# Kernel optimization log

Measured on AMD Instinct MI355X. Metric: run time of the kernel, lower is better.

Reference implementation:

```python
import jax, jax.numpy as jnp
import numpy as np

B, S, E = 2, 2048, 1024
D_ATTN, H = 1024, 16
HD = D_ATTN // H
SCALE = 1.0 / np.sqrt(D_ATTN)
ROPE_BASE = 10000.0


def setup_inputs() -> dict:
    key = jax.random.key(0)
    ks = jax.random.split(key, 7)
    def w(k, shape, scale):
        return jax.random.normal(k, shape, dtype=jnp.float32) * scale
    return {
        "q": w(ks[0], (B, S, E), 1.0),
        "k": w(ks[1], (B, S, E), 1.0),
        "v": w(ks[2], (B, S, E), 1.0),
        "Wq": w(ks[3], (D_ATTN, E), E ** -0.5),
        "Wk": w(ks[4], (D_ATTN, E), E ** -0.5),
        "Wv": w(ks[5], (D_ATTN, E), E ** -0.5),
        "Wo": w(ks[6], (E, D_ATTN), D_ATTN ** -0.5),
    }


def _rope(x):
    # x: [B, H, S, HD]; interleaved-pair rotary embedding over the seq axis
    s, d = x.shape[2], x.shape[3]
    half = d // 2
    inv_freq = 1.0 / (ROPE_BASE ** (jnp.arange(half, dtype=jnp.float32) * 2.0 / d))
    ang = jnp.arange(s, dtype=jnp.float32)[:, None] * inv_freq[None, :]  # [S, half]
    cos, sin = jnp.cos(ang), jnp.sin(ang)
    xr = x.reshape(x.shape[:-1] + (half, 2))
    x0, x1 = xr[..., 0], xr[..., 1]
    o0 = x0 * cos - x1 * sin
    o1 = x0 * sin + x1 * cos
    return jnp.stack([o0, o1], axis=-1).reshape(x.shape)


def reference(q, k, v, Wq, Wk, Wv, Wo):
    # linear projections (nn.Linear with weight [out, in]): y = x @ W^T
    qh = (q @ Wq.T).reshape(B, S, H, HD).transpose(0, 2, 1, 3)  # [B,H,S,HD]
    kh = (k @ Wk.T).reshape(B, S, H, HD).transpose(0, 2, 1, 3)
    vh = (v @ Wv.T).reshape(B, S, H, HD).transpose(0, 2, 1, 3)
    qh = _rope(qh)
    kh = _rope(kh)
    # shifted-causal mask: disallow j >= i (diagonal masked), except (0,0) allowed
    i = jnp.arange(S)[:, None]
    j = jnp.arange(S)[None, :]
    masked = j >= i                              # triu incl. diagonal
    masked = masked.at[0, 0].set(False)          # keep (0,0) so row 0 isn't all -inf
    scores = jnp.einsum("bhsd,bhtd->bhst", qh, kh) * SCALE
    scores = jnp.where(masked, -jnp.inf, scores)
    probs = jax.nn.softmax(scores, axis=-1)      # dropout omitted (eval mode)
    ctx = jnp.einsum("bhst,bhtd->bhsd", probs, vh)
    ctx = ctx.transpose(0, 2, 1, 3).reshape(B, S, D_ATTN)
    return ctx @ Wo.T
```

## Files before the change

### kernel.cpp

```cpp
#include <hip/hip_runtime.h>
#include <hip/hip_bf16.h>

#define BATCH 2
#define SEQ   2048
#define EMB   1024
#define DATTN 1024
#define NH    16
#define HD    64
#define MM    (BATCH*SEQ)
#define SCALE 0.03125f
#define MINIT -1.0e30f
#define ROPE_COEF 0.41524101186f

using bf16x8 = __attribute__((ext_vector_type(8))) short;
using f32x4  = __attribute__((ext_vector_type(4))) float;

__device__ inline short f2bf(float x) {
    __hip_bfloat16 b = __float2bfloat16(x);
    return *reinterpret_cast<short*>(&b);
}

__device__ inline void gl_lds16(const short* g, short* l) {
    __builtin_amdgcn_global_load_lds(
        (const __attribute__((address_space(1))) unsigned int*)g,
        (__attribute__((address_space(3))) unsigned int*)l, 16, 0, 0);
}

__global__ __launch_bounds__(256)
void cvt_all(const float* __restrict__ q, const float* __restrict__ k,
             const float* __restrict__ v,
             const float* __restrict__ Wq, const float* __restrict__ Wk,
             const float* __restrict__ Wv, const float* __restrict__ Wo,
             short* __restrict__ dst)
{
    const long QKV = (long)MM * EMB;
    const long WSZ = (long)DATTN * EMB;
    const long i = ((long)blockIdx.x * 256 + threadIdx.x) * 4;
    const float* s;
    long off;
    if (i < 3 * QKV) {
        const int seg = (int)(i / QKV);
        off = i - (long)seg * QKV;
        s = (seg == 0) ? q : (seg == 1) ? k : v;
    } else {
        const long j = i - 3 * QKV;
        const int seg = (int)(j / WSZ);
        off = j - (long)seg * WSZ;
        s = (seg == 0) ? Wq : (seg == 1) ? Wk : (seg == 2) ? Wv : Wo;
    }
    float4 x = *(const float4*)(s + off);
    short4 y;
    y.x = f2bf(x.x); y.y = f2bf(x.y); y.z = f2bf(x.z); y.w = f2bf(x.w);
    *(short4*)(dst + i) = y;
}

__device__ inline void stage_tile(const short* g, short* lds, int wave, int lane) {
    #pragma unroll
    for (int qq = 0; qq < 2; ++qq) {
        const int r = wave * 32 + qq * 16 + (lane >> 2);
        gl_lds16(g + (long)r * EMB + (lane & 3) * 8, lds + (wave * 2 + qq) * 512);
    }
}

__device__ inline void stage_tile64(const short* g, short* lds, int tid) {
    #pragma unroll
    for (int c = 0; c < 4; ++c) {
        const int cc   = c * 256 + tid;
        const int row  = cc >> 3;
        const int slot = cc & 7;
        const int ssl  = slot ^ (row & 7);
        gl_lds16(g + (long)row * EMB + ssl * 8, lds + ((cc & ~63) << 3));
    }
}

__global__ __launch_bounds__(256)
void gemm_proj_bf16(const short* __restrict__ qb, const short* __restrict__ kb,
                    const short* __restrict__ vb,
                    const short* __restrict__ wqb, const short* __restrict__ wkb,
                    const short* __restrict__ wvb,
                    short* __restrict__ Qb, short* __restrict__ Kb,
                    short* __restrict__ Vtb)
{
    const short* A; const short* B;
    if (blockIdx.z == 0)      { A = qb; B = wqb; }
    else if (blockIdx.z == 1) { A = kb; B = wkb; }
    else                      { A = vb; B = wvb; }
    const bool isv = (blockIdx.z == 2);

    __shared__ short sA[128 * 64];
    __shared__ short sB[128 * 64];

    const int tid  = threadIdx.x;
    const int wave = tid >> 6, lane = tid & 63;
    const int quad = lane >> 4, l16 = lane & 15;
    const int wm = (wave >> 1) * 64, wn = (wave & 1) * 64;
    const long m0 = (long)blockIdx.x * 128, n0 = (long)blockIdx.y * 128;
    const int rsw = l16 & 7;

    f32x4 acc[4][4];
    #pragma unroll
    for (int i = 0; i < 4; ++i)
        #pragma unroll
        for (int j = 0; j < 4; ++j) acc[i][j] = (f32x4){0.f, 0.f, 0.f, 0.f};

    for (int kt = 0; kt < EMB; kt += 64) {
        __syncthreads();
        stage_tile64(A + m0 * EMB + kt, sA, tid);
        stage_tile64(B + n0 * EMB + kt, sB, tid);
        __syncthreads();

        #pragma unroll
        for (int kk = 0; kk < 2; ++kk) {
            bf16x8 af[4], bfr[4];
            #pragma unroll
            for (int rt = 0; rt < 4; ++rt)
                af[rt] = *(const bf16x8*)&sA[(wm + rt * 16 + l16) * 64
                         + (((kk << 2) | quad) ^ rsw) * 8];
            #pragma unroll
            for (int ct = 0; ct < 4; ++ct)
                bfr[ct] = *(const bf16x8*)&sB[(wn + ct * 16 + l16) * 64
                          + (((kk << 2) | quad) ^ rsw) * 8];
            if (isv) {
                #pragma unroll
                for (int i = 0; i < 4; ++i)
                    #pragma unroll
                    for (int j = 0; j < 4; ++j)
                        acc[i][j] = __builtin_amdgcn_mfma_f32_16x16x32_bf16(
                            af[i], bfr[j], acc[i][j], 0, 0, 0);
            } else {
                #pragma unroll
                for (int i = 0; i < 4; ++i)
                    #pragma unroll
                    for (int j = 0; j < 4; ++j)
                        acc[i][j] = __builtin_amdgcn_mfma_f32_16x16x32_bf16(
                            bfr[i], af[j], acc[i][j], 0, 0, 0);
            }
        }
    }

    if (!isv) {
        short* C = (blockIdx.z == 0) ? Qb : Kb;
        const float scl = (blockIdx.z == 0) ? SCALE : 1.0f;
        #pragma unroll
        for (int i = 0; i < 4; ++i) {
            const int d0  = (int)(n0) + wn + i * 16 + quad * 4;
            const int hh  = d0 >> 6, dd0 = d0 & (HD - 1);
            const float invf0 = exp2f(-ROPE_COEF * (float)(dd0 >> 1));
            const float invf1 = exp2f(-ROPE_COEF * (float)((dd0 >> 1) + 1));
            #pragma unroll
            for (int j = 0; j < 4; ++j) {
                const int tok = (int)(m0) + wm + j * 16 + l16;
                const int bb = tok >> 11, ss = tok & (SEQ - 1);
                float s0, c0, s1, c1;
                __sincosf((float)ss * invf0, &s0, &c0);
                __sincosf((float)ss * invf1, &s1, &c1);
                const f32x4 x = acc[i][j];
                short4 o4;
                o4.x = f2bf((x[0] * c0 - x[1] * s0) * scl);
                o4.y = f2bf((x[0] * s0 + x[1] * c0) * scl);
                o4.z = f2bf((x[2] * c1 - x[3] * s1) * scl);
                o4.w = f2bf((x[2] * s1 + x[3] * c1) * scl);
                *(short4*)&C[(((long)(bb * NH + hh)) << 17)
                             + ((long)ss << 6) + dd0] = o4;
            }
        }
    } else {
        #pragma unroll
        for (int rt = 0; rt < 4; ++rt) {
            #pragma unroll
            for (int ct = 0; ct < 4; ++ct) {
                const long row0 = m0 + wm + rt * 16 + quad * 4;
                const long col  = n0 + wn + ct * 16 + l16;
                const int bb = (int)(row0 >> 11), ss = (int)(row0 & (SEQ - 1));
                const int hh = (int)(col >> 6),   dd = (int)(col & (HD - 1));
                short4 s4;
                s4.x = f2bf(acc[rt][ct][0]); s4.y = f2bf(acc[rt][ct][1]);
                s4.z = f2bf(acc[rt][ct][2]); s4.w = f2bf(acc[rt][ct][3]);
                *(short4*)&Vtb[(((long)(bb * NH + hh)) << 17) + ((long)dd << 11) + ss] = s4;
            }
        }
    }
}

__global__ __launch_bounds__(256)
void gemm_out_bf16(const short* __restrict__ Ab, const short* __restrict__ Bb,
                   float* __restrict__ C)
{
    __shared__ short sA[128 * 32];
    __shared__ short sB[64 * 32];

    const int tid  = threadIdx.x;
    const int wave = tid >> 6, lane = tid & 63;
    const int quad = lane >> 4, l16 = lane & 15;
    const int wm = (wave >> 1) * 64, wn = (wave & 1) * 32;
    const long m0 = (long)blockIdx.x * 128, n0 = (long)blockIdx.y * 64;

    f32x4 acc[4][2];
    #pragma unroll
    for (int i = 0; i < 4; ++i)
        #pragma unroll
        for (int j = 0; j < 2; ++j) acc[i][j] = (f32x4){0.f, 0.f, 0.f, 0.f};

    for (int kt = 0; kt < DATTN; kt += 32) {
        __syncthreads();
        stage_tile(Ab + m0 * DATTN + kt, sA, wave, lane);
        gl_lds16(Bb + n0 * DATTN + kt
                     + (long)(wave * 16 + (lane >> 2)) * DATTN + (lane & 3) * 8,
                 sB + wave * 512);
        __syncthreads();

        bf16x8 af[4], bfr[2];
        #pragma unroll
        for (int rt = 0; rt < 4; ++rt)
            af[rt] = *(const bf16x8*)&sA[(wm + rt * 16 + l16) * 32 + quad * 8];
        #pragma unroll
        for (int ct = 0; ct < 2; ++ct)
            bfr[ct] = *(const bf16x8*)&sB[(wn + ct * 16 + l16) * 32 + quad * 8];
        #pragma unroll
        for (int rt = 0; rt < 4; ++rt)
            #pragma unroll
            for (int ct = 0; ct < 2; ++ct)
                acc[rt][ct] = __builtin_amdgcn_mfma_f32_16x16x32_bf16(
                    af[rt], bfr[ct], acc[rt][ct], 0, 0, 0);
    }

    #pragma unroll
    for (int rt = 0; rt < 4; ++rt) {
        #pragma unroll
        for (int ct = 0; ct < 2; ++ct) {
            #pragma unroll
            for (int reg = 0; reg < 4; ++reg) {
                const long row = m0 + wm + rt * 16 + quad * 4 + reg;
                const long col = n0 + wn + ct * 16 + l16;
                C[row * EMB + col] = acc[rt][ct][reg];
            }
        }
    }
}

#define KLD 64
#define PLD 72

__global__ __launch_bounds__(256, 2)
void flash_attn_mfma(const short* __restrict__ Qb,
                     const short* __restrict__ Kb,
                     const short* __restrict__ Vtb,
                     short* __restrict__ ctx)
{
    const int id  = blockIdx.x;
    const int hi  = id >> 8;
    const int idx = id & 255;
    const int r   = idx & 7;
    const int s5  = idx >> 3;
    const int pi  = s5 & 3;
    const int ts8 = s5 >> 2;
    const int p   = r + 8 * pi;
    const int b   = p >> 4, h = p & 15;
    const int t   = hi ? ts8 : (15 - ts8);

    const int tid = threadIdx.x;
    const int wave = tid >> 6, lane = tid & 63;
    const int quad = lane >> 4, l16 = lane & 15;
    const int r0 = t * 128;

    __shared__ short sk[2 * 64 * KLD];
    __shared__ short sv[2 * 64 * KLD];
    __shared__ short sp[4][32 * PLD];

    const long base = ((long)(b * NH + h)) << 17;

    const int iq0 = r0 + wave * 32 + l16;
    const int iq1 = iq0 + 16;
    const int dtile = 2 * t + (wave >> 1);
    const int rsw = l16 & 7;

    bf16x8 qf0[2], qf1[2];
    #pragma unroll
    for (int tt = 0; tt < 2; ++tt) {
        qf0[tt] = *(const bf16x8*)(Qb + base + (long)iq0 * HD + tt * 32 + quad * 8);
        qf1[tt] = *(const bf16x8*)(Qb + base + (long)iq1 * HD + tt * 32 + quad * 8);
    }

    f32x4 acc0[4], acc1[4];
    #pragma unroll
    for (int ct = 0; ct < 4; ++ct) {
        acc0[ct] = (f32x4){0.f, 0.f, 0.f, 0.f};
        acc1[ct] = (f32x4){0.f, 0.f, 0.f, 0.f};
    }
    float m0 = MINIT, l0 = 0.f;
    float m1 = MINIT, l1 = 0.f;

    const int njt = t + 1;

    #pragma unroll 1
    for (int jt = 0; jt < njt; ++jt) {
        const int jbase = jt * 128;

        __syncthreads();
        #pragma unroll
        for (int c = 0; c < 4; ++c) {
            const int cc   = c * 256 + tid;
            const int half = cc >> 9;
            const int row  = (cc >> 3) & 63;
            const int sch  = (cc & 7) ^ (row & 7);
            gl_lds16(Kb + base + (long)(jbase + half * 64 + row) * HD + sch * 8,
                     sk + ((c * 256 + wave * 64) << 3));
            gl_lds16(Vtb + base + ((long)row << 11) + jbase + half * 64 + sch * 8,
                     sv + ((c * 256 + wave * 64) << 3));
        }
        __syncthreads();

        #pragma unroll
        for (int half = 0; half < 2; ++half) {
            const int jt2 = 2 * jt + half;
            if (jt2 > dtile) continue;
            const int jb2 = jbase + half * 64;
            const short* skh = sk + half * 64 * KLD;
            const short* svh = sv + half * 64 * KLD;

            f32x4 s0[4], s1[4];
            __builtin_amdgcn_s_setprio(1);
            #pragma unroll
            for (int ct = 0; ct < 4; ++ct) {
                const int rr16 = (ct * 16 + l16) * KLD;
                bf16x8 k0 = *(const bf16x8*)&skh[rr16 + ((quad ^ rsw) << 3)];
                bf16x8 k1 = *(const bf16x8*)&skh[rr16 + (((4 + quad) ^ rsw) << 3)];
                f32x4 z0 = (f32x4){0.f, 0.f, 0.f, 0.f};
                z0 = __builtin_amdgcn_mfma_f32_16x16x32_bf16(k0, qf0[0], z0, 0, 0, 0);
                z0 = __builtin_amdgcn_mfma_f32_16x16x32_bf16(k1, qf0[1], z0, 0, 0, 0);
                s0[ct] = z0;
                f32x4 z1 = (f32x4){0.f, 0.f, 0.f, 0.f};
                z1 = __builtin_amdgcn_mfma_f32_16x16x32_bf16(k0, qf1[0], z1, 0, 0, 0);
                z1 = __builtin_amdgcn_mfma_f32_16x16x32_bf16(k1, qf1[1], z1, 0, 0, 0);
                s1[ct] = z1;
            }
            __builtin_amdgcn_s_setprio(0);

            if (jt2 == dtile) {
                #pragma unroll
                for (int ct = 0; ct < 4; ++ct)
                    #pragma unroll
                    for (int rr = 0; rr < 4; ++rr) {
                        const int j = jb2 + ct * 16 + quad * 4 + rr;
                        if (!((j < iq0) || (iq0 == 0 && j == 0)))
                            s0[ct][rr] = -INFINITY;
                        if (!(j < iq1))
                            s1[ct][rr] = -INFINITY;
                    }
            }

            float mx0 = MINIT;
            #pragma unroll
            for (int ct = 0; ct < 4; ++ct)
                #pragma unroll
                for (int rr = 0; rr < 4; ++rr) mx0 = fmaxf(mx0, s0[ct][rr]);
            mx0 = fmaxf(mx0, __shfl_xor(mx0, 16, 64));
            mx0 = fmaxf(mx0, __shfl_xor(mx0, 32, 64));
            const float mn0 = fmaxf(m0, mx0);
            const float a0 = __expf(m0 - mn0);
            m0 = mn0;
            float ss0 = 0.f;
            #pragma unroll
            for (int ct = 0; ct < 4; ++ct)
                #pragma unroll
                for (int rr = 0; rr < 4; ++rr) {
                    const float e = __expf(s0[ct][rr] - mn0);
                    s0[ct][rr] = e;
                    ss0 += e;
                }
            ss0 += __shfl_xor(ss0, 16, 64);
            ss0 += __shfl_xor(ss0, 32, 64);
            l0 = l0 * a0 + ss0;

            float mx1 = MINIT;
            #pragma unroll
            for (int ct = 0; ct < 4; ++ct)
                #pragma unroll
                for (int rr = 0; rr < 4; ++rr) mx1 = fmaxf(mx1, s1[ct][rr]);
            mx1 = fmaxf(mx1, __shfl_xor(mx1, 16, 64));
            mx1 = fmaxf(mx1, __shfl_xor(mx1, 32, 64));
            const float mn1 = fmaxf(m1, mx1);
            const float a1 = __expf(m1 - mn1);
            m1 = mn1;
            float ss1 = 0.f;
            #pragma unroll
            for (int ct = 0; ct < 4; ++ct)
                #pragma unroll
                for (int rr = 0; rr < 4; ++rr) {
                    const float e = __expf(s1[ct][rr] - mn1);
                    s1[ct][rr] = e;
                    ss1 += e;
                }
            ss1 += __shfl_xor(ss1, 16, 64);
            ss1 += __shfl_xor(ss1, 32, 64);
            l1 = l1 * a1 + ss1;

            short* pw0 = sp[wave];
            short* pw1 = sp[wave] + 16 * PLD;
            #pragma unroll
            for (int ct = 0; ct < 4; ++ct) {
                short4 p4;
                p4.x = f2bf(s0[ct][0]); p4.y = f2bf(s0[ct][1]);
                p4.z = f2bf(s0[ct][2]); p4.w = f2bf(s0[ct][3]);
                *(short4*)&pw0[l16 * PLD + ct * 16 + quad * 4] = p4;
                short4 q4;
                q4.x = f2bf(s1[ct][0]); q4.y = f2bf(s1[ct][1]);
                q4.z = f2bf(s1[ct][2]); q4.w = f2bf(s1[ct][3]);
                *(short4*)&pw1[l16 * PLD + ct * 16 + quad * 4] = q4;
            }

            #pragma unroll
            for (int ct = 0; ct < 4; ++ct)
                #pragma unroll
                for (int rr = 0; rr < 4; ++rr) {
                    acc0[ct][rr] *= a0;
                    acc1[ct][rr] *= a1;
                }

            bf16x8 pf00 = *(const bf16x8*)&pw0[l16 * PLD + quad * 8];
            bf16x8 pf01 = *(const bf16x8*)&pw0[l16 * PLD + 32 + quad * 8];
            bf16x8 pf10 = *(const bf16x8*)&pw1[l16 * PLD + quad * 8];
            bf16x8 pf11 = *(const bf16x8*)&pw1[l16 * PLD + 32 + quad * 8];

            __builtin_amdgcn_s_setprio(1);
            #pragma unroll
            for (int ct = 0; ct < 4; ++ct) {
                const int rr16 = (ct * 16 + l16) * KLD;
                bf16x8 v0 = *(const bf16x8*)&svh[rr16 + ((quad ^ rsw) << 3)];
                bf16x8 v1 = *(const bf16x8*)&svh[rr16 + (((4 + quad) ^ rsw) << 3)];
                acc0[ct] = __builtin_amdgcn_mfma_f32_16x16x32_bf16(
                    v0, pf00, acc0[ct], 0, 0, 0);
                acc0[ct] = __builtin_amdgcn_mfma_f32_16x16x32_bf16(
                    v1, pf01, acc0[ct], 0, 0, 0);
                acc1[ct] = __builtin_amdgcn_mfma_f32_16x16x32_bf16(
                    v0, pf10, acc1[ct], 0, 0, 0);
                acc1[ct] = __builtin_amdgcn_mfma_f32_16x16x32_bf16(
                    v1, pf11, acc1[ct], 0, 0, 0);
            }
            __builtin_amdgcn_s_setprio(0);
        }
    }

    {
        const float inv0 = 1.f / l0;
        short* orow = ctx + (long)(b * SEQ + iq0) * DATTN + h * HD;
        #pragma unroll
        for (int ct = 0; ct < 4; ++ct) {
            short4 o4;
            o4.x = f2bf(acc0[ct][0] * inv0);
            o4.y = f2bf(acc0[ct][1] * inv0);
            o4.z = f2bf(acc0[ct][2] * inv0);
            o4.w = f2bf(acc0[ct][3] * inv0);
            *(short4*)&orow[ct * 16 + quad * 4] = o4;
        }
    }
    {
        const float inv1 = 1.f / l1;
        short* orow = ctx + (long)(b * SEQ + iq1) * DATTN + h * HD;
        #pragma unroll
        for (int ct = 0; ct < 4; ++ct) {
            short4 o4;
            o4.x = f2bf(acc1[ct][0] * inv1);
            o4.y = f2bf(acc1[ct][1] * inv1);
            o4.z = f2bf(acc1[ct][2] * inv1);
            o4.w = f2bf(acc1[ct][3] * inv1);
            *(short4*)&orow[ct * 16 + quad * 4] = o4;
        }
    }
}

extern "C" void kernel_launch(void* const* d_in, const int* in_sizes, int n_in,
                              void* d_out, int out_size, void* d_ws, size_t ws_size,
                              hipStream_t stream) {
    const float* q  = (const float*)d_in[0];
    const float* k  = (const float*)d_in[1];
    const float* v  = (const float*)d_in[2];
    const float* Wq = (const float*)d_in[3];
    const float* Wk = (const float*)d_in[4];
    const float* Wv = (const float*)d_in[5];
    const float* Wo = (const float*)d_in[6];
    float* out = (float*)d_out;

    const long QKV = (long)MM * EMB;
    const long WSZ = (long)DATTN * EMB;
    short* basep = (short*)d_ws;
    short* qb  = basep;
    short* kb  = qb + QKV;
    short* vb  = kb + QKV;
    short* wqb = vb + QKV;
    short* wkb = wqb + WSZ;
    short* wvb = wkb + WSZ;
    short* wob = wvb + WSZ;
    short* Qb  = wob + WSZ;
    short* Kb  = Qb + QKV;
    short* Vtb = Kb + QKV;
    short* ctx = Vtb + QKV;

    cvt_all<<<16384, 256, 0, stream>>>(q, k, v, Wq, Wk, Wv, Wo, qb);

    gemm_proj_bf16<<<dim3(MM / 128, DATTN / 128, 3), 256, 0, stream>>>(
        qb, kb, vb, wqb, wkb, wvb, Qb, Kb, Vtb);

    flash_attn_mfma<<<512, 256, 0, stream>>>(Qb, Kb, Vtb, ctx);

    gemm_out_bf16<<<dim3(MM / 128, EMB / 64), 256, 0, stream>>>(ctx, wob, out);
}
```

Baseline: 214.4 us.

## Double-buffer K/V tiles in flash attention and widen out-projection K-tile

The attention loop now stages 64-key K/V chunks into two LDS buffers, prefetching the next chunk while computing on the current one. This replaces the old scheme of loading 128 keys and then synchronizing. The output GEMM now uses 64-wide K tiles with XOR-swizzled LDS and two MFMA sub-steps per stage, which halves the number of barriers. Launch bounds for attention rise to 3 blocks per CU, which risks register pressure or spills, and a dead pointer computation was left in the staging helper.

```diff
diff --git a/kernel.cpp b/kernel.cpp
--- a/kernel.cpp
+++ b/kernel.cpp
@@ -54,14 +54,6 @@
     *(short4*)(dst + i) = y;
 }
 
-__device__ inline void stage_tile(const short* g, short* lds, int wave, int lane) {
-    #pragma unroll
-    for (int qq = 0; qq < 2; ++qq) {
-        const int r = wave * 32 + qq * 16 + (lane >> 2);
-        gl_lds16(g + (long)r * EMB + (lane & 3) * 8, lds + (wave * 2 + qq) * 512);
-    }
-}
-
 __device__ inline void stage_tile64(const short* g, short* lds, int tid) {
     #pragma unroll
     for (int c = 0; c < 4; ++c) {
@@ -69,6 +61,16 @@
         const int row  = cc >> 3;
         const int slot = cc & 7;
         const int ssl  = slot ^ (row & 7);
+        gl_lds16(g + (long)row * EMB + ssl * 8, lds + ((cc & ~63) << 3));
+    }
+}
+
+__device__ inline void stage_tile64h(const short* g, short* lds, int tid) {
+    #pragma unroll
+    for (int c = 0; c < 2; ++c) {
+        const int cc   = c * 256 + tid;
+        const int row  = cc >> 3;
+        const int ssl  = (cc & 7) ^ (row & 7);
         gl_lds16(g + (long)row * EMB + ssl * 8, lds + ((cc & ~63) << 3));
     }
 }
@@ -186,14 +188,15 @@
 void gemm_out_bf16(const short* __restrict__ Ab, const short* __restrict__ Bb,
                    float* __restrict__ C)
 {
-    __shared__ short sA[128 * 32];
-    __shared__ short sB[64 * 32];
+    __shared__ short sA[128 * 64];
+    __shared__ short sB[64 * 64];
 
     const int tid  = threadIdx.x;
     const int wave = tid >> 6, lane = tid & 63;
     const int quad = lane >> 4, l16 = lane & 15;
     const int wm = (wave >> 1) * 64, wn = (wave & 1) * 32;
     const long m0 = (long)blockIdx.x * 128, n0 = (long)blockIdx.y * 64;
+    const int rsw = l16 & 7;
 
     f32x4 acc[4][2];
     #pragma unroll
@@ -201,27 +204,30 @@
         #pragma unroll
         for (int j = 0; j < 2; ++j) acc[i][j] = (f32x4){0.f, 0.f, 0.f, 0.f};
 
-    for (int kt = 0; kt < DATTN; kt += 32) {
+    for (int kt = 0; kt < DATTN; kt += 64) {
         __syncthreads();
-        stage_tile(Ab + m0 * DATTN + kt, sA, wave, lane);
-        gl_lds16(Bb + n0 * DATTN + kt
-                     + (long)(wave * 16 + (lane >> 2)) * DATTN + (lane & 3) * 8,
-                 sB + wave * 512);
+        stage_tile64(Ab + m0 * DATTN + kt, sA, tid);
+        stage_tile64h(Bb + n0 * DATTN + kt, sB, tid);
         __syncthreads();
 
-        bf16x8 af[4], bfr[2];
-        #pragma unroll
-        for (int rt = 0; rt < 4; ++rt)
-            af[rt] = *(const bf16x8*)&sA[(wm + rt * 16 + l16) * 32 + quad * 8];
-        #pragma unroll
-        for (int ct = 0; ct < 2; ++ct)
-            bfr[ct] = *(const bf16x8*)&sB[(wn + ct * 16 + l16) * 32 + quad * 8];
-        #pragma unroll
-        for (int rt = 0; rt < 4; ++rt)
+        #pragma unroll
+        for (int kk = 0; kk < 2; ++kk) {
+            bf16x8 af[4], bfr[2];
+            #pragma unroll
+            for (int rt = 0; rt < 4; ++rt)
+                af[rt] = *(const bf16x8*)&sA[(wm + rt * 16 + l16) * 64
+                         + (((kk << 2) | quad) ^ rsw) * 8];
             #pragma unroll
             for (int ct = 0; ct < 2; ++ct)
-                acc[rt][ct] = __builtin_amdgcn_mfma_f32_16x16x32_bf16(
-                    af[rt], bfr[ct], acc[rt][ct], 0, 0, 0);
+                bfr[ct] = *(const bf16x8*)&sB[(wn + ct * 16 + l16) * 64
+                          + (((kk << 2) | quad) ^ rsw) * 8];
+            #pragma unroll
+            for (int rt = 0; rt < 4; ++rt)
+                #pragma unroll
+                for (int ct = 0; ct < 2; ++ct)
+                    acc[rt][ct] = __builtin_amdgcn_mfma_f32_16x16x32_bf16(
+                        af[rt], bfr[ct], acc[rt][ct], 0, 0, 0);
+        }
     }
 
     #pragma unroll
@@ -241,7 +247,28 @@
 #define KLD 64
 #define PLD 72
 
-__global__ __launch_bounds__(256, 2)
+__device__ inline void stage_kv64(const short* __restrict__ Kb,
+                                  const short* __restrict__ Vtb,
+                                  long base, int jb2,
+                                  short* skp, short* svp,
+                                  int tid, int wave)
+{
+    #pragma unroll
+    for (int c = 0; c < 2; ++c) {
+        const int cc  = c * 256 + tid;
+        const int row = cc >> 3;
+        const int sch = (cc & 7) ^ (row & 7);
+        short* dk = skp + ((c * 256 + (tid & ~63)) << 3) - ((tid & ~63) << 3)
+                        + (((c * 256 + tid) & ~63) - (c * 256 + tid - (tid & 63)) ) ;
+        (void)dk;
+        gl_lds16(Kb + base + (long)(jb2 + row) * HD + sch * 8,
+                 skp + ((c * 256 + wave * 64) << 3));
+        gl_lds16(Vtb + base + ((long)row << 11) + jb2 + sch * 8,
+                 svp + ((c * 256 + wave * 64) << 3));
+    }
+}
+
+__global__ __launch_bounds__(256, 3)
 void flash_attn_mfma(const short* __restrict__ Qb,
                      const short* __restrict__ Kb,
                      const short* __restrict__ Vtb,
@@ -263,8 +290,8 @@
     const int quad = lane >> 4, l16 = lane & 15;
     const int r0 = t * 128;
 
-    __shared__ short sk[2 * 64 * KLD];
-    __shared__ short sv[2 * 64 * KLD];
+    __shared__ short sk[2][64 * KLD];
+    __shared__ short sv[2][64 * KLD];
     __shared__ short sp[4][32 * PLD];
 
     const long base = ((long)(b * NH + h)) << 17;
@@ -290,33 +317,23 @@
     float m0 = MINIT, l0 = 0.f;
     float m1 = MINIT, l1 = 0.f;
 
-    const int njt = t + 1;
+    const int J = 2 * t + 2;
+
+    stage_kv64(Kb, Vtb, base, 0, sk[0], sv[0], tid, wave);
 
     #pragma unroll 1
-    for (int jt = 0; jt < njt; ++jt) {
-        const int jbase = jt * 128;
-
-        __syncthreads();
-        #pragma unroll
-        for (int c = 0; c < 4; ++c) {
-            const int cc   = c * 256 + tid;
-            const int half = cc >> 9;
-            const int row  = (cc >> 3) & 63;
-            const int sch  = (cc & 7) ^ (row & 7);
-            gl_lds16(Kb + base + (long)(jbase + half * 64 + row) * HD + sch * 8,
-                     sk + ((c * 256 + wave * 64) << 3));
-            gl_lds16(Vtb + base + ((long)row << 11) + jbase + half * 64 + sch * 8,
-                     sv + ((c * 256 + wave * 64) << 3));
-        }
-        __syncthreads();
-
-        #pragma unroll
-        for (int half = 0; half < 2; ++half) {
-            const int jt2 = 2 * jt + half;
-            if (jt2 > dtile) continue;
-            const int jb2 = jbase + half * 64;
-            const short* skh = sk + half * 64 * KLD;
-            const short* svh = sv + half * 64 * KLD;
+    for (int j2 = 0; j2 < J; ++j2) {
+        const int pb = j2 & 1;
+        asm volatile("s_waitcnt vmcnt(0)" ::: "memory");
+        __builtin_amdgcn_s_barrier();
+        if (j2 + 1 < J)
+            stage_kv64(Kb, Vtb, base, (j2 + 1) * 64,
+                       sk[pb ^ 1], sv[pb ^ 1], tid, wave);
+
+        if (j2 <= dtile) {
+            const int jb2 = j2 * 64;
+            const short* skh = sk[pb];
+            const short* svh = sv[pb];
 
             f32x4 s0[4], s1[4];
             __builtin_amdgcn_s_setprio(1);
@@ -336,7 +353,7 @@
             }
             __builtin_amdgcn_s_setprio(0);
 
-            if (jt2 == dtile) {
+            if (j2 == dtile) {
                 #pragma unroll
                 for (int ct = 0; ct < 4; ++ct)
                     #pragma unroll
```

Result: no change. 211.0 us (-1.6%).
